# Optimization experiments

Hardware: AMD Instinct MI355X
Metric: run time of the kernel (lower is better)

## Reference

```python
import jax, jax.numpy as jnp
import numpy as np

B, N, DIM, H, DH = 8, 1024, 512, 8, 64
INNER = H * DH
SCALE = DH ** -0.5


def setup_inputs() -> dict:
    key = jax.random.key(0)
    ks = jax.random.split(key, 9)
    s = 0.02
    return {
        "x": jax.random.normal(ks[0], (B, N, DIM), jnp.float32),
        "lidar": jax.random.normal(ks[1], (B, N, INNER), jnp.float32),
        "w_qkv": jax.random.normal(ks[2], (3 * INNER, DIM), jnp.float32) * s,
        "w_merge": jax.random.normal(ks[3], (DH, DH), jnp.float32) * s,
        "b_merge": jnp.zeros((DH,), jnp.float32),
        "w_out": jax.random.normal(ks[4], (DIM, INNER), jnp.float32) * s,
        "b_out": jnp.zeros((DIM,), jnp.float32),
        "conv_w": jax.random.normal(ks[5], (2,), jnp.float32) * 0.5,
        "conv_b": jnp.zeros((), jnp.float32),
    }


def _split_heads(t):  # [b, n, h*d] -> [b, h, n, d]
    b, n, _ = t.shape
    return t.reshape(b, n, H, DH).transpose(0, 2, 1, 3)


def reference(x, lidar, w_qkv, w_merge, b_merge, w_out, b_out, conv_w, conv_b):
    b, n, _ = x.shape
    qkv = x @ w_qkv.T  # [b, n, 3*inner]
    q, k, v = jnp.split(qkv, 3, axis=-1)
    q, k, v = _split_heads(q), _split_heads(k), _split_heads(v)
    lid = _split_heads(lidar)

    dots = jnp.einsum('bhid,bhjd->bhij', q, k) * SCALE
    lidar_sim = jnp.einsum('bhid,bhjd->bhij', lid, lid) * SCALE
    lidar_sim = jax.nn.softmax(lidar_sim, axis=-1)

    # 1x1 conv over 2 channels == learned linear blend of the two score maps
    mid = conv_w[0] * dots + conv_w[1] * lidar_sim + conv_b
    attn = jax.nn.softmax(mid, axis=-1)

    out = jnp.einsum('bhij,bhjd->bhid', attn, v)
    out = out @ w_merge.T + b_merge                  # per-head linear_merge
    out = out.transpose(0, 2, 1, 3).reshape(b, n, INNER)  # b h n d -> b n (h d)
    out = out @ w_out.T + b_out                      # to_out (dropout = identity)
    return (out, lidar)
```

## Files before the change

### kernel.cpp

```cpp
#include <hip/hip_runtime.h>
#include <hip/hip_bf16.h>

#define B_      8
#define N_      1024
#define DIM_    512
#define H_      8
#define DH_     64
#define INNER_  512
#define SCALE_  0.125f
#define LOG2E_  1.4426950408889634f

typedef __attribute__((ext_vector_type(8))) __bf16         bf16x8;
typedef __attribute__((ext_vector_type(8))) unsigned short ushort8;
typedef __attribute__((ext_vector_type(4))) float          f32x4;

union FragCast { ushort8 u; bf16x8 b; };
union FragU32  { unsigned int u[4]; bf16x8 b; };

__device__ inline bf16x8 ld_frag(const unsigned short* p) {
    FragCast f; f.u = *(const ushort8*)p; return f.b;
}

__device__ inline f32x4 mfma16(bf16x8 a, bf16x8 b, f32x4 c) {
    return __builtin_amdgcn_mfma_f32_16x16x32_bf16(a, b, c, 0, 0, 0);
}

__device__ inline float fexp2(float x) { return __builtin_amdgcn_exp2f(x); }

__device__ inline unsigned short f2bf(float x) {
    unsigned int u = __float_as_uint(x);
    unsigned int lsb = (u >> 16) & 1u;
    u += 0x7fffu + lsb;
    return (unsigned short)(u >> 16);
}

__device__ inline unsigned int pack_bf2(float hi, float lo) {
    return __builtin_amdgcn_perm(__float_as_uint(hi), __float_as_uint(lo), 0x07060302u);
}

__device__ inline void gl_lds(const unsigned short* g, unsigned short* l) {
    __builtin_amdgcn_global_load_lds(
        (const __attribute__((address_space(1))) unsigned int*)g,
        (__attribute__((address_space(3))) unsigned int*)l, 16, 0, 0);
}

__global__ __launch_bounds__(256) void k_convert(
    const float* __restrict__ x, const float* __restrict__ lidar,
    const float* __restrict__ wqkv, const float* __restrict__ wmerge,
    const float* __restrict__ wout,
    unsigned short* __restrict__ x_bf, unsigned short* __restrict__ lid_bf,
    float* __restrict__ out_lidar,
    unsigned short* __restrict__ wqkv_bf, unsigned short* __restrict__ wm_bf,
    unsigned short* __restrict__ wout_bf)
{
    const int bx = blockIdx.x, tid = threadIdx.x;
    const float* src; unsigned short* dst; bool isLid = false; long base;
    if (bx < 1024)      { src = x;      dst = x_bf;    base = (long)bx * 1024; }
    else if (bx < 2048) { src = lidar;  dst = lid_bf;  base = (long)(bx - 1024) * 1024; isLid = true; }
    else if (bx < 2240) { src = wqkv;   dst = wqkv_bf; base = (long)(bx - 2048) * 1024; }
    else if (bx < 2304) { src = wout;   dst = wout_bf; base = (long)(bx - 2240) * 1024; }
    else                { src = wmerge; dst = wm_bf;   base = 0; }
    for (int k = 0; k < 4; k++) {
        long j = base + k * 256 + tid;
        float4 v = ((const float4*)src)[j];
        ushort4 o;
        o.x = f2bf(v.x); o.y = f2bf(v.y); o.z = f2bf(v.z); o.w = f2bf(v.w);
        ((ushort4*)dst)[j] = o;
        if (isLid) ((float4*)out_lidar)[j] = v;
    }
}

__global__ __launch_bounds__(256) void k_gemm_qkv(
    const unsigned short* __restrict__ A, const unsigned short* __restrict__ Bm,
    unsigned short* __restrict__ C, unsigned short* __restrict__ vt,
    int M, int Nd, int K)
{
    __shared__ unsigned short sMem[128 * 136];
    unsigned short* sA = sMem;
    unsigned short* sB = sMem + 128 * 64;
    const int tid  = threadIdx.x;
    const int lane = tid & 63, wave = tid >> 6;
    const int q = lane >> 4, l15 = lane & 15, l7 = l15 & 7;
    const int xq0 = (q ^ l7) << 3, xq4 = ((q + 4) ^ l7) << 3;
    const int m0 = blockIdx.x * 128, n0 = blockIdx.y * 128;
    const int wm = (wave >> 1) * 64, wn = (wave & 1) * 64;
    f32x4 acc[4][4] = {};

    for (int k0 = 0; k0 < K; k0 += 64) {
        __syncthreads();
        for (int i = 0; i < 4; i++) {
            int c = i * 256 + tid;
            int row = c >> 3;
            int gcol = ((c & 7) ^ (row & 7)) << 3;
            gl_lds(&A[(long)(m0 + row) * K + k0 + gcol], &sA[c * 8]);
            gl_lds(&Bm[(long)(n0 + row) * K + k0 + gcol], &sB[c * 8]);
        }
        __syncthreads();
        for (int kk = 0; kk < 2; kk++) {
            const int xx = kk ? xq4 : xq0;
            bf16x8 af[4], bfr[4];
            for (int i = 0; i < 4; i++)
                af[i]  = ld_frag(&sA[(wm + i * 16 + l15) * 64 + xx]);
            for (int i = 0; i < 4; i++)
                bfr[i] = ld_frag(&sB[(wn + i * 16 + l15) * 64 + xx]);
            for (int mi = 0; mi < 4; mi++)
                for (int ni = 0; ni < 4; ni++)
                    acc[mi][ni] = mfma16(af[mi], bfr[ni], acc[mi][ni]);
        }
    }
    if (n0 < 1024) {
        for (int mi = 0; mi < 4; mi++)
            for (int ni = 0; ni < 4; ni++)
                for (int r = 0; r < 4; r++) {
                    int row = m0 + wm + mi * 16 + q * 4 + r;
                    int col = n0 + wn + ni * 16 + l15;
                    C[(long)row * Nd + col] = f2bf(acc[mi][ni][r]);
                }
    } else {
        __syncthreads();
        for (int mi = 0; mi < 4; mi++) {
            int t0 = wm + mi * 16 + q * 4;
            for (int ni = 0; ni < 4; ni++) {
                int f = wn + ni * 16 + l15;
                ushort4 o4;
                o4.x = f2bf(acc[mi][ni][0]); o4.y = f2bf(acc[mi][ni][1]);
                o4.z = f2bf(acc[mi][ni][2]); o4.w = f2bf(acc[mi][ni][3]);
                *(ushort4*)&sMem[f * 136 + t0] = o4;
            }
        }
        __syncthreads();
        const long fb = (long)(n0 - 1024) * (B_ * N_) + m0;
        for (int i = 0; i < 8; i++) {
            int g = i * 256 + tid;
            int f = g >> 4, grp = g & 15;
            int base = (grp >> 2) * 32 + (grp & 3) * 4;
            ushort4 a4 = *(const ushort4*)&sMem[f * 136 + base];
            ushort4 b4 = *(const ushort4*)&sMem[f * 136 + base + 16];
            ushort8 o8 = {a4.x, a4.y, a4.z, a4.w, b4.x, b4.y, b4.z, b4.w};
            *(ushort8*)&vt[fb + (long)f * (B_ * N_) + grp * 8] = o8;
        }
    }
}

__global__ __launch_bounds__(256) void k_gemm_out(
    const unsigned short* __restrict__ A, const unsigned short* __restrict__ Bm,
    const float* __restrict__ bias, float* __restrict__ C, int M, int Nd, int K)
{
    __shared__ unsigned short sA[128 * 64];
    __shared__ unsigned short sB[64 * 64];
    const int tid  = threadIdx.x;
    const int lane = tid & 63, wave = tid >> 6;
    const int q = lane >> 4, l15 = lane & 15, l7 = l15 & 7;
    const int xq0 = (q ^ l7) << 3, xq4 = ((q + 4) ^ l7) << 3;
    const int m0 = blockIdx.x * 128, n0 = blockIdx.y * 64;
    const int wm = (wave >> 1) * 64, wn = (wave & 1) * 32;
    f32x4 acc[4][2] = {};

    for (int k0 = 0; k0 < K; k0 += 64) {
        __syncthreads();
        for (int i = 0; i < 4; i++) {
            int c = i * 256 + tid;
            int row = c >> 3;
            int gcol = ((c & 7) ^ (row & 7)) << 3;
            gl_lds(&A[(long)(m0 + row) * K + k0 + gcol], &sA[c * 8]);
            if (i < 2)
                gl_lds(&Bm[(long)(n0 + row) * K + k0 + gcol], &sB[c * 8]);
        }
        __syncthreads();
        for (int kk = 0; kk < 2; kk++) {
            const int xx = kk ? xq4 : xq0;
            bf16x8 af[4], bfr[2];
            for (int i = 0; i < 4; i++)
                af[i]  = ld_frag(&sA[(wm + i * 16 + l15) * 64 + xx]);
            for (int i = 0; i < 2; i++)
                bfr[i] = ld_frag(&sB[(wn + i * 16 + l15) * 64 + xx]);
            for (int mi = 0; mi < 4; mi++)
                for (int ni = 0; ni < 2; ni++)
                    acc[mi][ni] = mfma16(af[mi], bfr[ni], acc[mi][ni]);
        }
    }
    for (int mi = 0; mi < 4; mi++)
        for (int ni = 0; ni < 2; ni++)
            for (int r = 0; r < 4; r++) {
                int row = m0 + wm + mi * 16 + q * 4 + r;
                int col = n0 + wn + ni * 16 + l15;
                C[(long)row * Nd + col] = acc[mi][ni][r] + bias[col];
            }
}

__global__ __launch_bounds__(512) void k_flash(
    const unsigned short* __restrict__ qkv_bf, const unsigned short* __restrict__ lid_bf,
    const unsigned short* __restrict__ vt,
    const unsigned short* __restrict__ wm_bf, const float* __restrict__ b_merge,
    const float* __restrict__ conv_w, const float* __restrict__ conv_b,
    unsigned short* __restrict__ tmp_bf)
{
    __shared__ unsigned short smem[3 * 64 * 64];
    __shared__ float sRS[8][16];
    unsigned short* sK   = smem;
    unsigned short* sLid = smem + 4096;
    unsigned short* sVT  = smem + 8192;

    const int tid = threadIdx.x, lane = tid & 63, wave = tid >> 6;
    const int q = lane >> 4, l15 = lane & 15, l7 = l15 & 7;
    const int xq0 = (q ^ l7) << 3, xq4 = ((q + 4) ^ l7) << 3;
    const int bh = blockIdx.x, ipair = blockIdx.y;
    const int b = bh >> 3, h = bh & 7;
    const int i0w = ipair * 128 + wave * 16;
    const long rowB = (long)b * N_;
    const int colh = h * DH_;
    const float k0c = conv_w[0] * SCALE_ * LOG2E_;
    const float k2c = conv_b[0] * LOG2E_;
    const float c1L = conv_w[1] * LOG2E_;
    const float sc = SCALE_ * LOG2E_;

    const int srow = tid >> 3;
    const int sgc  = ((tid & 7) ^ (srow & 7)) << 3;
    unsigned short* dK = &sK[tid * 8];
    unsigned short* dL = &sLid[tid * 8];
    unsigned short* dV = &sVT[tid * 8];
    const unsigned short* gK = &qkv_bf[(rowB + srow) * 1536 + 512 + colh + sgc];
    const unsigned short* gL = &lid_bf[(rowB + srow) * INNER_ + colh + sgc];
    const unsigned short* gV = &vt[(long)(colh + srow) * (B_ * N_) + rowB + sgc];

    unsigned short* dL1a = &smem[tid * 8];
    unsigned short* dL1b = &smem[(512 + tid) * 8];
    const unsigned short* gL1a = &lid_bf[(rowB + srow) * INNER_ + colh + sgc];
    const unsigned short* gL1b = &lid_bf[(rowB + 64 + srow) * INNER_ + colh + sgc];

    const unsigned short* sR[8];
#pragma unroll
    for (int ns = 0; ns < 8; ns++) sR[ns] = &smem[(ns * 16 + l15) * 64];

    bf16x8 qf[2], lfq[2];
#pragma unroll
    for (int ks = 0; ks < 2; ks++) {
        qf[ks]  = ld_frag(&qkv_bf[(rowB + i0w + l15) * 1536 + colh + ks * 32 + q * 8]);
        lfq[ks] = ld_frag(&lid_bf[(rowB + i0w + l15) * INNER_ + colh + ks * 32 + q * 8]);
    }

    float rsl = 0.f;
    for (int j0 = 0; j0 < N_; j0 += 128) {
        __syncthreads();
        gl_lds(gL1a, dL1a);
        gl_lds(gL1b, dL1b);
        gL1a += 128 * INNER_; gL1b += 128 * INNER_;
        __syncthreads();
#pragma unroll
        for (int ns = 0; ns < 8; ns++) {
            f32x4 cv = {0.f, 0.f, 0.f, 0.f};
            cv = mfma16(ld_frag(sR[ns] + xq0), lfq[0], cv);
            cv = mfma16(ld_frag(sR[ns] + xq4), lfq[1], cv);
            for (int r = 0; r < 4; r++) rsl += fexp2(cv[r] * sc);
        }
    }
    rsl += __shfl_xor(rsl, 16);
    rsl += __shfl_xor(rsl, 32);
    const float k1 = c1L / rsl;

    float rs = 0.f;
    f32x4 o[4] = {};

    for (int j0 = 0; j0 < N_; j0 += 64) {
        __syncthreads();
        gl_lds(gK, dK); gl_lds(gL, dL); gl_lds(gV, dV);
        gK += 64 * 1536; gL += 64 * INNER_; gV += 64;
        __syncthreads();

#pragma unroll
        for (int ns2 = 0; ns2 < 2; ns2++) {
            FragU32 fa;
#pragma unroll
            for (int h2 = 0; h2 < 2; h2++) {
                int ns = ns2 * 2 + h2;
                f32x4 a = {0.f, 0.f, 0.f, 0.f};
                a = mfma16(ld_frag(sR[ns] + xq0), qf[0], a);
                a = mfma16(ld_frag(sR[ns] + xq4), qf[1], a);
                f32x4 cv = {0.f, 0.f, 0.f, 0.f};
                cv = mfma16(ld_frag(sR[ns + 4] + xq0), lfq[0], cv);
                cv = mfma16(ld_frag(sR[ns + 4] + xq4), lfq[1], cv);
                float pv[4];
                for (int r = 0; r < 4; r++) {
                    float els = fexp2(cv[r] * sc);
                    float t = fmaf(k0c, a[r], k2c);
                    t = fmaf(k1, els, t);
                    pv[r] = fexp2(t);
                    rs += pv[r];
                }
                fa.u[h2 * 2 + 0] = pack_bf2(pv[1], pv[0]);
                fa.u[h2 * 2 + 1] = pack_bf2(pv[3], pv[2]);
            }
#pragma unroll
            for (int dt = 0; dt < 4; dt++) {
                int vrow = dt * 16 + l15;
                bf16x8 vb = ld_frag(&sVT[vrow * 64 + (((ns2 * 4 + q) ^ l7) << 3)]);
                o[dt] = mfma16(fa.b, vb, o[dt]);
            }
        }
    }

    rs += __shfl_xor(rs, 16);
    rs += __shfl_xor(rs, 32);
    if (q == 0) sRS[wave][l15] = rs;
    float invr[4];
    for (int r = 0; r < 4; r++) invr[r] = 1.f / sRS[wave][q * 4 + r];

    __syncthreads();
    unsigned short* pO = &smem[wave * 16 * 72];
#pragma unroll
    for (int dt = 0; dt < 4; dt++)
        for (int r = 0; r < 4; r++)
            pO[(q * 4 + r) * 72 + dt * 16 + l15] = f2bf(o[dt][r] * invr[r]);

    f32x4 mo[4] = {};
#pragma unroll
    for (int ks = 0; ks < 2; ks++) {
        bf16x8 af = ld_frag(&pO[l15 * 72 + ks * 32 + q * 8]);
#pragma unroll
        for (int ns = 0; ns < 4; ns++) {
            bf16x8 wf = ld_frag(&wm_bf[(ns * 16 + l15) * 64 + ks * 32 + q * 8]);
            mo[ns] = mfma16(af, wf, mo[ns]);
        }
    }
#pragma unroll
    for (int ns = 0; ns < 4; ns++) {
        float bm = b_merge[ns * 16 + l15];
        for (int r = 0; r < 4; r++) {
            long row = rowB + i0w + q * 4 + r;
            tmp_bf[row * INNER_ + colh + ns * 16 + l15] = f2bf(mo[ns][r] + bm);
        }
    }
}

extern "C" void kernel_launch(void* const* d_in, const int* in_sizes, int n_in,
                              void* d_out, int out_size, void* d_ws, size_t ws_size,
                              hipStream_t stream) {
    const float* x       = (const float*)d_in[0];
    const float* lidar   = (const float*)d_in[1];
    const float* w_qkv   = (const float*)d_in[2];
    const float* w_merge = (const float*)d_in[3];
    const float* b_merge = (const float*)d_in[4];
    const float* w_out   = (const float*)d_in[5];
    const float* b_out   = (const float*)d_in[6];
    const float* conv_w  = (const float*)d_in[7];
    const float* conv_b  = (const float*)d_in[8];

    float* out0      = (float*)d_out;
    float* out_lidar = out0 + (long)B_ * N_ * INNER_;

    size_t off = 0;
    auto carve = [&](size_t bytes) {
        void* p = (char*)d_ws + off;
        off += (bytes + 255) & ~(size_t)255;
        return p;
    };
    unsigned short* qkv_bf  = (unsigned short*)carve((size_t)B_ * N_ * 3 * INNER_ * 2);
    unsigned short* lid_bf  = (unsigned short*)carve((size_t)B_ * N_ * INNER_ * 2);
    unsigned short* x_bf    = (unsigned short*)carve((size_t)B_ * N_ * DIM_ * 2);
    unsigned short* wqkv_bf = (unsigned short*)carve((size_t)3 * INNER_ * DIM_ * 2);
    unsigned short* wout_bf = (unsigned short*)carve((size_t)DIM_ * INNER_ * 2);
    unsigned short* wm_bf   = (unsigned short*)carve((size_t)DH_ * DH_ * 2);
    unsigned short* tmp_bf  = (unsigned short*)carve((size_t)B_ * N_ * INNER_ * 2);
    unsigned short* vt_bf   = (unsigned short*)carve((size_t)INNER_ * B_ * N_ * 2);

    k_convert<<<2305, 256, 0, stream>>>(x, lidar, w_qkv, w_merge, w_out,
                                        x_bf, lid_bf, out_lidar,
                                        wqkv_bf, wm_bf, wout_bf);

    k_gemm_qkv<<<dim3(64, 12), 256, 0, stream>>>(
        x_bf, wqkv_bf, qkv_bf, vt_bf, B_ * N_, 3 * INNER_, DIM_);

    k_flash<<<dim3(64, 8), 512, 0, stream>>>(
        qkv_bf, lid_bf, vt_bf, wm_bf, b_merge, conv_w, conv_b, tmp_bf);

    k_gemm_out<<<dim3(64, 8), 256, 0, stream>>>(
        tmp_bf, wout_bf, b_out, out0, B_ * N_, DIM_, INNER_);
}
```

Baseline: 179.0 us.

## Double-buffer LDS loads in flash kernel with explicit waitcnt and barriers

Both passes of the flash kernel (the lidar row-sum pass and the main attention pass) now use two LDS buffers. The next tile's global_load_lds is issued before computing on the current one, with explicit vmcnt waits and raw s_barrier in place of paired __syncthreads. The compute bodies move into templates with compile-time LDS offsets, and s_setprio raises priority during the MFMA sections. This is meant to hide global-to-LDS latency behind compute, at the cost of doubling LDS use to 48KB per block and relying on hand-counted vmcnt values.

```diff
diff --git a/kernel.cpp b/kernel.cpp
--- a/kernel.cpp
+++ b/kernel.cpp
@@ -43,6 +43,14 @@
         (const __attribute__((address_space(1))) unsigned int*)g,
         (__attribute__((address_space(3))) unsigned int*)l, 16, 0, 0);
 }
+
+#define BARF() do { asm volatile("" ::: "memory"); \
+                    __builtin_amdgcn_s_barrier();  \
+                    asm volatile("" ::: "memory"); } while (0)
+#define WAITV(n) asm volatile("s_waitcnt vmcnt(" #n ")" ::: "memory")
+
+#define KEEP8(x) do { FragU32 _k; _k.b = (x); \
+    asm volatile("" :: "v"(_k.u[0]), "v"(_k.u[1]), "v"(_k.u[2]), "v"(_k.u[3])); } while (0)
 
 __global__ __launch_bounds__(256) void k_convert(
     const float* __restrict__ x, const float* __restrict__ lidar,
@@ -188,6 +196,58 @@
             }
 }
 
+
+template <int SB>
+__device__ __forceinline__ void comp1(const unsigned short* smem, int a0, int a4,
+                                      const bf16x8* lfq, float sc, float& rsl)
+{
+#pragma unroll
+    for (int ns = 0; ns < 8; ns++) {
+        f32x4 cv = {0.f, 0.f, 0.f, 0.f};
+        cv = mfma16(ld_frag(&smem[SB + ns * 1024 + a0]), lfq[0], cv);
+        cv = mfma16(ld_frag(&smem[SB + ns * 1024 + a4]), lfq[1], cv);
+#pragma unroll
+        for (int r = 0; r < 4; r++) rsl += fexp2(cv[r] * sc);
+    }
+}
+
+template <int KB, int LB, int VB>
+__device__ __forceinline__ void comp2(const unsigned short* smem, int a0, int a4,
+                                      const bf16x8* qf, const bf16x8* lfq,
+                                      float k0c, float k2c, float k1, float sc,
+                                      float& rs, f32x4* o)
+{
+#pragma unroll
+    for (int ns2 = 0; ns2 < 2; ns2++) {
+        FragU32 fa;
+#pragma unroll
+        for (int h2 = 0; h2 < 2; h2++) {
+            const int ns = ns2 * 2 + h2;
+            f32x4 a = {0.f, 0.f, 0.f, 0.f};
+            a = mfma16(ld_frag(&smem[KB + ns * 1024 + a0]), qf[0], a);
+            a = mfma16(ld_frag(&smem[KB + ns * 1024 + a4]), qf[1], a);
+            f32x4 cv = {0.f, 0.f, 0.f, 0.f};
+            cv = mfma16(ld_frag(&smem[LB + ns * 1024 + a0]), lfq[0], cv);
+            cv = mfma16(ld_frag(&smem[LB + ns * 1024 + a4]), lfq[1], cv);
+            float pv[4];
+#pragma unroll
+            for (int r = 0; r < 4; r++) {
+                float els = fexp2(cv[r] * sc);
+                float t = fmaf(k0c, a[r], k2c);
+                t = fmaf(k1, els, t);
+                pv[r] = fexp2(t);
+                rs += pv[r];
+            }
+            fa.u[h2 * 2 + 0] = pack_bf2(pv[1], pv[0]);
+            fa.u[h2 * 2 + 1] = pack_bf2(pv[3], pv[2]);
+        }
+        const int av = ns2 ? a4 : a0;
+#pragma unroll
+        for (int dt = 0; dt < 4; dt++)
+            o[dt] = mfma16(fa.b, ld_frag(&smem[VB + dt * 1024 + av]), o[dt]);
+    }
+}
+
 __global__ __launch_bounds__(512) void k_flash(
     const unsigned short* __restrict__ qkv_bf, const unsigned short* __restrict__ lid_bf,
     const unsigned short* __restrict__ vt,
@@ -195,15 +255,13 @@
     const float* __restrict__ conv_w, const float* __restrict__ conv_b,
     unsigned short* __restrict__ tmp_bf)
 {
-    __shared__ unsigned short smem[3 * 64 * 64];
+    __shared__ unsigned short smem[24576];
     __shared__ float sRS[8][16];
-    unsigned short* sK   = smem;
-    unsigned short* sLid = smem + 4096;
-    unsigned short* sVT  = smem + 8192;
 
     const int tid = threadIdx.x, lane = tid & 63, wave = tid >> 6;
     const int q = lane >> 4, l15 = lane & 15, l7 = l15 & 7;
     const int xq0 = (q ^ l7) << 3, xq4 = ((q + 4) ^ l7) << 3;
+    const int a0 = l15 * 64 + xq0, a4 = l15 * 64 + xq4;
     const int bh = blockIdx.x, ipair = blockIdx.y;
     const int b = bh >> 3, h = bh & 7;
     const int i0w = ipair * 128 + wave * 16;
@@ -216,21 +274,22 @@
 
     const int srow = tid >> 3;
     const int sgc  = ((tid & 7) ^ (srow & 7)) << 3;
-    unsigned short* dK = &sK[tid * 8];
-    unsigned short* dL = &sLid[tid * 8];
-    unsigned short* dV = &sVT[tid * 8];
+    unsigned short* dK0 = &smem[0     + tid * 8];
+    unsigned short* dL0 = &smem[4096  + tid * 8];
+    unsigned short* dV0 = &smem[8192  + tid * 8];
+    unsigned short* dK1 = &smem[12288 + tid * 8];
+    unsigned short* dL1 = &smem[16384 + tid * 8];
+    unsigned short* dV1 = &smem[20480 + tid * 8];
     const unsigned short* gK = &qkv_bf[(rowB + srow) * 1536 + 512 + colh + sgc];
     const unsigned short* gL = &lid_bf[(rowB + srow) * INNER_ + colh + sgc];
     const unsigned short* gV = &vt[(long)(colh + srow) * (B_ * N_) + rowB + sgc];
 
-    unsigned short* dL1a = &smem[tid * 8];
-    unsigned short* dL1b = &smem[(512 + tid) * 8];
+    unsigned short* dA0 = &smem[0     + tid * 8];
+    unsigned short* dB0 = &smem[4096  + tid * 8];
+    unsigned short* dA1 = &smem[8192  + tid * 8];
+    unsigned short* dB1 = &smem[12288 + tid * 8];
     const unsigned short* gL1a = &lid_bf[(rowB + srow) * INNER_ + colh + sgc];
     const unsigned short* gL1b = &lid_bf[(rowB + 64 + srow) * INNER_ + colh + sgc];
-
-    const unsigned short* sR[8];
-#pragma unroll
-    for (int ns = 0; ns < 8; ns++) sR[ns] = &smem[(ns * 16 + l15) * 64];
 
     bf16x8 qf[2], lfq[2];
 #pragma unroll
@@ -238,21 +297,30 @@
         qf[ks]  = ld_frag(&qkv_bf[(rowB + i0w + l15) * 1536 + colh + ks * 32 + q * 8]);
         lfq[ks] = ld_frag(&lid_bf[(rowB + i0w + l15) * INNER_ + colh + ks * 32 + q * 8]);
     }
+    KEEP8(qf[0]); KEEP8(qf[1]); KEEP8(lfq[0]); KEEP8(lfq[1]);
+    WAITV(0);
+
+#define ISS1(dA, dB) do { gl_lds(gL1a, dA); gl_lds(gL1b, dB); \
+                          gL1a += 128 * INNER_; gL1b += 128 * INNER_; } while (0)
+#define ISS2(dK, dL, dV) do { gl_lds(gK, dK); gl_lds(gL, dL); gl_lds(gV, dV); \
+                              gK += 64 * 1536; gL += 64 * INNER_; gV += 64; } while (0)
 
     float rsl = 0.f;
-    for (int j0 = 0; j0 < N_; j0 += 128) {
-        __syncthreads();
-        gl_lds(gL1a, dL1a);
-        gl_lds(gL1b, dL1b);
-        gL1a += 128 * INNER_; gL1b += 128 * INNER_;
-        __syncthreads();
-#pragma unroll
-        for (int ns = 0; ns < 8; ns++) {
-            f32x4 cv = {0.f, 0.f, 0.f, 0.f};
-            cv = mfma16(ld_frag(sR[ns] + xq0), lfq[0], cv);
-            cv = mfma16(ld_frag(sR[ns] + xq4), lfq[1], cv);
-            for (int r = 0; r < 4; r++) rsl += fexp2(cv[r] * sc);
-        }
+    ISS1(dA0, dB0);
+    for (int s = 0; s < 4; s++) {
+        ISS1(dA1, dB1);
+        WAITV(2); BARF();
+        __builtin_amdgcn_s_setprio(1);
+        comp1<0>(smem, a0, a4, lfq, sc, rsl);
+        __builtin_amdgcn_s_setprio(0);
+        BARF();
+        if (s < 3) { ISS1(dA0, dB0); WAITV(2); }
+        else       { WAITV(0); }
+        BARF();
+        __builtin_amdgcn_s_setprio(1);
+        comp1<8192>(smem, a0, a4, lfq, sc, rsl);
+        __builtin_amdgcn_s_setprio(0);
+        BARF();
     }
     rsl += __shfl_xor(rsl, 16);
     rsl += __shfl_xor(rsl, 32);
@@ -261,43 +329,24 @@
     float rs = 0.f;
     f32x4 o[4] = {};
 
-    for (int j0 = 0; j0 < N_; j0 += 64) {
-        __syncthreads();
-        gl_lds(gK, dK); gl_lds(gL, dL); gl_lds(gV, dV);
-        gK += 64 * 1536; gL += 64 * INNER_; gV += 64;
-        __syncthreads();
-
-#pragma unroll
-        for (int ns2 = 0; ns2 < 2; ns2++) {
-            FragU32 fa;
-#pragma unroll
-            for (int h2 = 0; h2 < 2; h2++) {
-                int ns = ns2 * 2 + h2;
-                f32x4 a = {0.f, 0.f, 0.f, 0.f};
-                a = mfma16(ld_frag(sR[ns] + xq0), qf[0], a);
-                a = mfma16(ld_frag(sR[ns] + xq4), qf[1], a);
-                f32x4 cv = {0.f, 0.f, 0.f, 0.f};
-                cv = mfma16(ld_frag(sR[ns + 4] + xq0), lfq[0], cv);
-                cv = mfma16(ld_frag(sR[ns + 4] + xq4), lfq[1], cv);
-                float pv[4];
-                for (int r = 0; r < 4; r++) {
-                    float els = fexp2(cv[r] * sc);
-                    float t = fmaf(k0c, a[r], k2c);
-                    t = fmaf(k1, els, t);
-                    pv[r] = fexp2(t);
-                    rs += pv[r];
-                }
-                fa.u[h2 * 2 + 0] = pack_bf2(pv[1], pv[0]);
-                fa.u[h2 * 2 + 1] = pack_bf2(pv[3], pv[2]);
-            }
-#pragma unroll
-            for (int dt = 0; dt < 4; dt++) {
-                int vrow = dt * 16 + l15;
-                bf16x8 vb = ld_frag(&sVT[vrow * 64 + (((ns2 * 4 + q) ^ l7) << 3)]);
-                o[dt] = mfma16(fa.b, vb, o[dt]);
-            }
-        }
-    }
+    ISS2(dK0, dL0, dV0);
+    for (int s = 0; s < 8; s++) {
+        ISS2(dK1, dL1, dV1);
+        WAITV(3); BARF();
+        __builtin_amdgcn_s_setprio(1);
+        comp2<0, 4096, 8192>(smem, a0, a4, qf, lfq, k0c, k2c, k1, sc, rs, o);
+        __builtin_amdgcn_s_setprio(0);
+        BARF();
+        if (s < 7) { ISS2(dK0, dL0, dV0); WAITV(3); }
+        else       { WAITV(0); }
+        BARF();
+        __builtin_amdgcn_s_setprio(1);
+        comp2<12288, 16384, 20480>(smem, a0, a4, qf, lfq, k0c, k2c, k1, sc, rs, o);
+        __builtin_amdgcn_s_setprio(0);
+        BARF();
+    }
+#undef ISS1
+#undef ISS2
 
     rs += __shfl_xor(rs, 16);
     rs += __shfl_xor(rs, 32);
@@ -305,7 +354,6 @@
     float invr[4];
     for (int r = 0; r < 4; r++) invr[r] = 1.f / sRS[wave][q * 4 + r];
 
-    __syncthreads();
     unsigned short* pO = &smem[wave * 16 * 72];
 #pragma unroll
     for (int dt = 0; dt < 4; dt++)
```

Result: no change. 178.9 us (-0.1%).
